# Kernel optimization log

Hardware: AMD Instinct MI355X
Metric: run time of the kernel (lower is better)

The kernel has to match this reference:

```python
import jax, jax.numpy as jnp
import numpy as np

N_GRAPHS = 1024   # pool of learnable adjacency blocks (len(Adjs))
BLOCK = 128       # nodes per graph (block size)
BATCH = 1024      # len(batch_idrange); D = BATCH * BLOCK rows
FEAT = 32         # input feature dim


def setup_inputs() -> dict:
    key = jax.random.key(0)
    k1, k2, k3 = jax.random.split(key, 3)
    # learnable per-graph adjacency weights (self.weights stacked)
    weights = jax.random.normal(k1, (N_GRAPHS, BLOCK, BLOCK), dtype=jnp.float32)
    # dense node-feature input [D, F] with D = BATCH * BLOCK
    inp = jax.random.normal(k2, (BATCH * BLOCK, FEAT), dtype=jnp.float32)
    # which adjacency block each batch element uses
    batch_idrange = jax.random.randint(k3, (BATCH,), 0, N_GRAPHS, dtype=jnp.int64)
    return {"input": inp, "weights": weights, "batch_idrange": batch_idrange}


def reference(input, weights, batch_idrange):
    # Original: blockdiag(weights[batch_idrange]) @ input.
    # Block-diagonal structure means each block only touches its own row slab,
    # so this is exactly a batched per-block matmul (same math, no zero padding).
    B = batch_idrange.shape[0]
    n = weights.shape[1]
    W = weights[batch_idrange]                    # [B, n, n] gather (irregular access)
    xb = input.reshape(B, n, -1)                  # [B, n, F]
    out = jnp.einsum('bij,bjf->bif', W, xb)       # [B, n, F]
    return out.reshape(input.shape[0], -1)        # [D, F]
```

## Files before the change

kernel.cpp:

```cpp
#include <hip/hip_runtime.h>

#define NODES 128
#define FEAT  32
#define XPAD  136

typedef __attribute__((ext_vector_type(8))) short bf16x8;
typedef __attribute__((ext_vector_type(4))) float f32x4;

typedef const __attribute__((address_space(1))) void gvoid;
typedef __attribute__((address_space(3))) void       svoid;

__device__ __forceinline__ unsigned pk_bf16(float a, float b) {
    unsigned ua = __builtin_bit_cast(unsigned, a);
    unsigned ub = __builtin_bit_cast(unsigned, b);
    ua += 0x7fffu + ((ua >> 16) & 1u);
    ub += 0x7fffu + ((ub >> 16) & 1u);
    return (ua >> 16) | (ub & 0xffff0000u);
}

__device__ __forceinline__ bf16x8 cvt_frag(float4 lo, float4 hi) {
    union { unsigned u[4]; bf16x8 v; } r;
    r.u[0] = pk_bf16(lo.x, lo.y);
    r.u[1] = pk_bf16(lo.z, lo.w);
    r.u[2] = pk_bf16(hi.x, hi.y);
    r.u[3] = pk_bf16(hi.z, hi.w);
    return r.v;
}

__global__ __launch_bounds__(512, 6)
void blockdiag_mm(const float* __restrict__ inp,
                  const float* __restrict__ weights,
                  const int* __restrict__ idx,
                  float* __restrict__ out)
{
    __shared__ __align__(16) float4 wc[NODES * 16];
    __shared__ __align__(16) short  xt[FEAT * XPAD];

    const int b  = blockIdx.x;
    const int u  = threadIdx.x;
    const int w  = u >> 6;
    const int l  = u & 63;
    const int ln = l & 15;
    const int q  = l >> 4;

    const float* __restrict__ xin = inp + (size_t)b * (NODES * FEAT);
    const float* __restrict__ wb  = weights + (size_t)idx[b] * (NODES * NODES);

    const float4* x4 = (const float4*)xin;
    const int fq = u & 7;
    const int k0 = (u >> 3) * 2;
    const float4 v0 = x4[k0 * 8 + fq];
    const float4 v1 = x4[(k0 + 1) * 8 + fq];

    auto stage_w = [&](int p) {
        #pragma unroll
        for (int s = 0; s < 4; ++s) {
            const int i    = s * 512 + u;
            const int row  = i >> 4;
            const int lseg = i & 15;
            const int gseg = (lseg - row) & 15;
            gvoid* g   = (gvoid*)(wb + row * NODES + p * 64 + gseg * 4);
            svoid* dst = (svoid*)(wc + s * 512 + w * 64);
            __builtin_amdgcn_global_load_lds(g, dst, 16, 0, 0);
        }
    };

    stage_w(0);

    {
        const float pv0[4] = {v0.x, v0.y, v0.z, v0.w};
        const float pv1[4] = {v1.x, v1.y, v1.z, v1.w};
        #pragma unroll
        for (int i = 0; i < 4; ++i)
            *(unsigned*)(&xt[(fq * 4 + i) * XPAD + k0]) = pk_bf16(pv0[i], pv1[i]);
    }
    __syncthreads();

    f32x4 acc[2] = {};
    const int arow = 16 * w + ln;

    #pragma unroll
    for (int p = 0; p < 2; ++p) {
        if (p == 1) {
            __syncthreads();
            stage_w(1);
            __syncthreads();
        }
        #pragma unroll
        for (int kcp = 0; kcp < 2; ++kcp) {
            const int kb = 2 * p + kcp;
            const int g0 = kcp * 8 + q * 2;
            const float4 alo = wc[arow * 16 + ((g0 + 0 + arow) & 15)];
            const float4 ahi = wc[arow * 16 + ((g0 + 1 + arow) & 15)];
            const bf16x8 afr = cvt_frag(alo, ahi);
            #pragma unroll
            for (int nt = 0; nt < 2; ++nt) {
                const bf16x8 bfr = *(const bf16x8*)(&xt[(16 * nt + ln) * XPAD + kb * 32 + q * 8]);
                acc[nt] = __builtin_amdgcn_mfma_f32_16x16x32_bf16(afr, bfr, acc[nt], 0, 0, 0);
            }
        }
    }

    float* ob = out + (size_t)b * (NODES * FEAT);
    #pragma unroll
    for (int nt = 0; nt < 2; ++nt)
        #pragma unroll
        for (int reg = 0; reg < 4; ++reg)
            ob[(16 * w + q * 4 + reg) * FEAT + 16 * nt + ln] = acc[nt][reg];
}

extern "C" void kernel_launch(void* const* d_in, const int* in_sizes, int n_in,
                              void* d_out, int out_size, void* d_ws, size_t ws_size,
                              hipStream_t stream) {
    const float* inp = (const float*)d_in[0];
    const float* wts = (const float*)d_in[1];
    const int*   idx = (const int*)d_in[2];
    float* outp = (float*)d_out;
    const int B = in_sizes[2];
    hipLaunchKernelGGL(blockdiag_mm, dim3(B), dim3(512), 0, stream,
                       inp, wts, idx, outp);
}
```

Before: 109.7 us.

## Load weight fragments directly into registers instead of staging through LDS

Drops the global_load_lds staging of the 128x128 weight block into shared memory. Each lane now reads its MFMA A-fragment straight from global memory as eight float4 loads, all issued up front. This removes the LDS buffer and two of the three block barriers, and the remaining barrier becomes a raw s_barrier that waits only on LDS. Each lane's global reads are now 32-byte chunks spread over rows rather than the previously coalesced row streams, so coalescing may suffer, and register pressure rises under launch_bounds(512,6).

Result: no change. 111.2 us (+1.4%).

```diff
diff --git a/kernel.cpp b/kernel.cpp
--- a/kernel.cpp
+++ b/kernel.cpp
@@ -6,9 +6,6 @@
 
 typedef __attribute__((ext_vector_type(8))) short bf16x8;
 typedef __attribute__((ext_vector_type(4))) float f32x4;
-
-typedef const __attribute__((address_space(1))) void gvoid;
-typedef __attribute__((address_space(3))) void       svoid;
 
 __device__ __forceinline__ unsigned pk_bf16(float a, float b) {
     unsigned ua = __builtin_bit_cast(unsigned, a);
@@ -33,8 +30,7 @@
                   const int* __restrict__ idx,
                   float* __restrict__ out)
 {
-    __shared__ __align__(16) float4 wc[NODES * 16];
-    __shared__ __align__(16) short  xt[FEAT * XPAD];
+    __shared__ __align__(16) short xt[FEAT * XPAD];
 
     const int b  = blockIdx.x;
     const int u  = threadIdx.x;
@@ -52,20 +48,14 @@
     const float4 v0 = x4[k0 * 8 + fq];
     const float4 v1 = x4[(k0 + 1) * 8 + fq];
 
-    auto stage_w = [&](int p) {
-        #pragma unroll
-        for (int s = 0; s < 4; ++s) {
-            const int i    = s * 512 + u;
-            const int row  = i >> 4;
-            const int lseg = i & 15;
-            const int gseg = (lseg - row) & 15;
-            gvoid* g   = (gvoid*)(wb + row * NODES + p * 64 + gseg * 4);
-            svoid* dst = (svoid*)(wc + s * 512 + w * 64);
-            __builtin_amdgcn_global_load_lds(g, dst, 16, 0, 0);
-        }
-    };
-
-    stage_w(0);
+    const float4* w4 = (const float4*)wb;
+    const int wbase = (16 * w + ln) * 32 + q * 2;
+    float4 wf[8];
+    #pragma unroll
+    for (int kb = 0; kb < 4; ++kb) {
+        wf[2 * kb + 0] = w4[wbase + kb * 8 + 0];
+        wf[2 * kb + 1] = w4[wbase + kb * 8 + 1];
+    }
 
     {
         const float pv0[4] = {v0.x, v0.y, v0.z, v0.w};
@@ -74,30 +64,20 @@
         for (int i = 0; i < 4; ++i)
             *(unsigned*)(&xt[(fq * 4 + i) * XPAD + k0]) = pk_bf16(pv0[i], pv1[i]);
     }
-    __syncthreads();
+
+    __builtin_amdgcn_sched_barrier(0);
+    asm volatile("s_waitcnt lgkmcnt(0)" ::: "memory");
+    __builtin_amdgcn_s_barrier();
+    __builtin_amdgcn_sched_barrier(0);
 
     f32x4 acc[2] = {};
-    const int arow = 16 * w + ln;
-
     #pragma unroll
-    for (int p = 0; p < 2; ++p) {
-        if (p == 1) {
-            __syncthreads();
-            stage_w(1);
-            __syncthreads();
-        }
+    for (int kb = 0; kb < 4; ++kb) {
+        const bf16x8 afr = cvt_frag(wf[2 * kb + 0], wf[2 * kb + 1]);
         #pragma unroll
-        for (int kcp = 0; kcp < 2; ++kcp) {
-            const int kb = 2 * p + kcp;
-            const int g0 = kcp * 8 + q * 2;
-            const float4 alo = wc[arow * 16 + ((g0 + 0 + arow) & 15)];
-            const float4 ahi = wc[arow * 16 + ((g0 + 1 + arow) & 15)];
-            const bf16x8 afr = cvt_frag(alo, ahi);
-            #pragma unroll
-            for (int nt = 0; nt < 2; ++nt) {
-                const bf16x8 bfr = *(const bf16x8*)(&xt[(16 * nt + ln) * XPAD + kb * 32 + q * 8]);
-                acc[nt] = __builtin_amdgcn_mfma_f32_16x16x32_bf16(afr, bfr, acc[nt], 0, 0, 0);
-            }
+        for (int nt = 0; nt < 2; ++nt) {
+            const bf16x8 bfr = *(const bf16x8*)(&xt[(16 * nt + ln) * XPAD + kb * 32 + q * 8]);
+            acc[nt] = __builtin_amdgcn_mfma_f32_16x16x32_bf16(afr, bfr, acc[nt], 0, 0, 0);
         }
     }
 
```
